# Kernel optimization log

Measured on AMD Instinct MI355X. Metric: run time of the kernel, lower is better.

## Reference

```python
import jax, jax.numpy as jnp
import numpy as np

EPS = 1e-12  # F.normalize default eps


def _l2_normalize(x, axis):
    n = jnp.sqrt(jnp.sum(x * x, axis=axis, keepdims=True))
    return x / jnp.maximum(n, EPS)


def setup_inputs() -> dict:
    key = jax.random.key(0)
    k1, k2 = jax.random.split(key)
    code = jax.random.normal(k1, (8, 768, 32, 32), dtype=jnp.float32)
    clusters = jax.random.normal(k2, (64, 768), dtype=jnp.float32)
    return {"code": code, "clusters": clusters, "image_hw": 512}


def reference(code, clusters, image_hw):
    # L2-normalize cluster centroids over channel dim and features over C
    normed_clusters = _l2_normalize(clusters, axis=1)            # [N, C]
    normed_features = _l2_normalize(code, axis=1)                # [B, C, H, W]
    # cosine similarity to every cluster
    inner_products = jnp.einsum('bchw,nc->bnhw', normed_features, normed_clusters)  # [B,N,H,W]
    # hard nearest-cluster assignment -> one-hot over N (channel axis 1)
    assign = jnp.argmax(inner_products, axis=1)                  # [B, H, W] int
    n_classes = clusters.shape[0]
    cluster_probs = jnp.moveaxis(
        jax.nn.one_hot(assign, n_classes, dtype=jnp.float32), -1, 1)  # [B,N,H,W]
    # training loss: negative mean of selected (max) similarity
    cluster_loss = -jnp.mean(jnp.sum(cluster_probs * inner_products, axis=1))
    # resize_to(cluster_probs, image): bilinear upsample to image resolution
    B, N = cluster_probs.shape[0], cluster_probs.shape[1]
    resized = jax.image.resize(cluster_probs, (B, N, image_hw, image_hw), method='bilinear')
    return (cluster_loss, resized, code)
```

## Files before the change

### kernel.cpp

```cpp
#include <hip/hip_runtime.h>

#define CCH 768
#define NCL 64
#define HWIN 1024
#define RES_ELEMS 134217728LL
#define CODE_ELEMS 6291456LL
#define CQUADS 1572863LL
#define COPY_BLOCKS 1536
#define DENSE_BLOCKS 2048

__global__ __launch_bounds__(256) void k_norm(const float* __restrict__ clusters,
                                              const float* __restrict__ code,
                                              float* __restrict__ nc_t,
                                              float* __restrict__ out)
{
    int tid = threadIdx.x;
    int n = blockIdx.x;
    __shared__ float red[256];
    float v0 = clusters[n * CCH + tid];
    float v1 = clusters[n * CCH + tid + 256];
    float v2 = clusters[n * CCH + tid + 512];
    red[tid] = v0 * v0 + v1 * v1 + v2 * v2;
    __syncthreads();
    for (int off = 128; off > 0; off >>= 1) {
        if (tid < off) red[tid] += red[tid + off];
        __syncthreads();
    }
    float scale = 1.0f / fmaxf(sqrtf(red[0]), 1e-12f);
    nc_t[(tid      ) * NCL + n] = v0 * scale;
    nc_t[(tid + 256) * NCL + n] = v1 * scale;
    nc_t[(tid + 512) * NCL + n] = v2 * scale;
    if (n == 0 && tid == 0) {
        out[0] = 0.0f;
        out[RES_ELEMS + 1] = code[0];
        out[RES_ELEMS + 2] = code[1];
        out[RES_ELEMS + 3] = code[2];
        out[RES_ELEMS + CODE_ELEMS] = code[CODE_ELEMS - 1];
    }
}

__global__ __launch_bounds__(256) void k_assign(const float* __restrict__ code,
                                                const float* __restrict__ nc_t,
                                                int* __restrict__ assign,
                                                float* __restrict__ out)
{
    __shared__ float lds_nc[64 * 64];
    __shared__ float lds_red[8 * 2048];
    __shared__ float lds_sq[8 * 32];

    int tid = threadIdx.x;
    int blk = blockIdx.x;
    int cg = tid >> 5;
    int ng = (tid >> 3) & 3;
    int pg = tid & 7;
    int b = blk >> 5;
    int pixb = (blk & 31) << 5;
    const float* codeB = code + (size_t)b * CCH * HWIN + pixb + (pg << 2);

    float acc[4][16];
    #pragma unroll
    for (int p = 0; p < 4; ++p)
        #pragma unroll
        for (int q = 0; q < 16; ++q) acc[p][q] = 0.f;
    float sq0 = 0.f, sq1 = 0.f, sq2 = 0.f, sq3 = 0.f;

    for (int k = 0; k < 12; ++k) {
        __syncthreads();
        const float4* src = (const float4*)(nc_t + k * 4096);
        float4* dst = (float4*)lds_nc;
        #pragma unroll
        for (int i = 0; i < 4; ++i) dst[tid + 256 * i] = src[tid + 256 * i];
        __syncthreads();
        #pragma unroll
        for (int m = 0; m < 8; ++m) {
            int ch = k * 64 + cg * 8 + m;
            float4 f = *(const float4*)(codeB + ch * HWIN);
            sq0 += f.x * f.x; sq1 += f.y * f.y; sq2 += f.z * f.z; sq3 += f.w * f.w;
            const float* ncrow = lds_nc + ((cg * 8 + m) << 6) + (ng << 4);
            #pragma unroll
            for (int q = 0; q < 16; ++q) {
                float w = ncrow[q];
                acc[0][q] += f.x * w;
                acc[1][q] += f.y * w;
                acc[2][q] += f.z * w;
                acc[3][q] += f.w * w;
            }
        }
    }

    #pragma unroll
    for (int p = 0; p < 4; ++p) {
        float4* dstp = (float4*)&lds_red[cg * 2048 + (pg * 4 + p) * 64 + ng * 16];
        dstp[0] = make_float4(acc[p][0],  acc[p][1],  acc[p][2],  acc[p][3]);
        dstp[1] = make_float4(acc[p][4],  acc[p][5],  acc[p][6],  acc[p][7]);
        dstp[2] = make_float4(acc[p][8],  acc[p][9],  acc[p][10], acc[p][11]);
        dstp[3] = make_float4(acc[p][12], acc[p][13], acc[p][14], acc[p][15]);
    }
    if (ng == 0) {
        lds_sq[cg * 32 + pg * 4 + 0] = sq0;
        lds_sq[cg * 32 + pg * 4 + 1] = sq1;
        lds_sq[cg * 32 + pg * 4 + 2] = sq2;
        lds_sq[cg * 32 + pg * 4 + 3] = sq3;
    }
    __syncthreads();

    for (int idx = tid; idx < 2048; idx += 256) {
        float s = 0.f;
        #pragma unroll
        for (int c2 = 0; c2 < 8; ++c2) s += lds_red[c2 * 2048 + idx];
        lds_nc[idx] = s;
    }
    __syncthreads();

    if (tid < 32) {
        float ss = 0.f;
        #pragma unroll
        for (int c2 = 0; c2 < 8; ++c2) ss += lds_sq[c2 * 32 + tid];
        float inv = 1.0f / fmaxf(sqrtf(ss), 1e-12f);
        float best = -1e30f; int bi = 0;
        for (int n = 0; n < 64; ++n) {
            float v = lds_nc[tid * 64 + n];
            if (v > best) { best = v; bi = n; }
        }
        assign[blk * 32 + tid] = bi;
        float l = best * inv;
        l += __shfl_down(l, 16);
        l += __shfl_down(l, 8);
        l += __shfl_down(l, 4);
        l += __shfl_down(l, 2);
        l += __shfl_down(l, 1);
        if (tid == 0) atomicAdd(out, -l * (1.0f / 8192.0f));
    }
}

__global__ __launch_bounds__(256) void k_dense(const int* __restrict__ assign,
                                               const float* __restrict__ code,
                                               float* __restrict__ out)
{
    int tid = threadIdx.x;
    int blk = blockIdx.x;

    if (blk >= DENSE_BLOCKS) {
        long long u = (long long)(blk - DENSE_BLOCKS) * 256 + tid;
        #pragma unroll
        for (int k = 0; k < 4; ++k) {
            long long q = u + (long long)k * (COPY_BLOCKS * 256);
            if (q < CQUADS) {
                const float* src = code + 3 + 4 * q;
                float4 v = make_float4(src[0], src[1], src[2], src[3]);
                *(float4*)(out + RES_ELEMS + 4 + 4 * q) = v;
            }
        }
        return;
    }

    int b =  blk >> 8;
    int n = (blk >> 2) & 63;
    int c =  blk & 3;
    int I0 = c << 7;
    int rbase = (I0 >> 4) - 1;

    __shared__ unsigned s_mask[10];
    __shared__ int4   s_jj[128];
    __shared__ float4 s_fj[128];

    int lane = tid & 63;
    int w = tid >> 6;

    {
        int r = (w << 1) + (lane >> 5);
        int ir = rbase + r; ir = ir < 0 ? 0 : (ir > 31 ? 31 : ir);
        bool pred = assign[(b << 10) + (ir << 5) + (lane & 31)] == n;
        unsigned long long m = __ballot(pred);
        if (lane == 0) { s_mask[(w << 1)] = (unsigned)m; s_mask[(w << 1) + 1] = (unsigned)(m >> 32); }
    }
    if (w == 0) {
        int r = 8 + (lane >> 5);
        int ir = rbase + r; ir = ir < 0 ? 0 : (ir > 31 ? 31 : ir);
        bool pred = assign[(b << 10) + (ir << 5) + (lane & 31)] == n;
        unsigned long long m = __ballot(pred);
        if (lane == 0) { s_mask[8] = (unsigned)m; s_mask[9] = (unsigned)(m >> 32); }
    }

    if (tid < 128) {
        int s = tid;
        int jl[4];
        if (s == 0) { jl[0] = 0; jl[1] = 1; jl[2] = 2; jl[3] = 511; }
        else { jl[0] = 4 * s - 1; jl[1] = 4 * s; jl[2] = 4 * s + 1; jl[3] = 4 * s + 2; }
        int pj[4]; float fjv[4];
        #pragma unroll
        for (int k = 0; k < 4; ++k) {
            int j = jl[k];
            float xj = (j + 0.5f) * 0.0625f - 0.5f;
            float fjf = floorf(xj);
            int jj = (int)fjf;
            fjv[k] = xj - fjf;
            int j0 = jj < 0 ? 0 : jj;
            int j1 = (jj + 1) > 31 ? 31 : (jj + 1);
            pj[k] = j0 | (j1 << 8);
        }
        s_jj[s] = make_int4(pj[0], pj[1], pj[2], pj[3]);
        s_fj[s] = make_float4(fjv[0], fjv[1], fjv[2], fjv[3]);
    }
    __syncthreads();

    int rr = tid >> 7;
    int s  = tid & 127;
    int4   pj4 = s_jj[s];
    float4 fj4 = s_fj[s];
    int   j0a[4] = { pj4.x & 255, pj4.y & 255, pj4.z & 255, pj4.w & 255 };
    int   j1a[4] = { pj4.x >> 8,  pj4.y >> 8,  pj4.z >> 8,  pj4.w >> 8 };
    float fja[4] = { fj4.x, fj4.y, fj4.z, fj4.w };

    long long planebase = 1LL + ((long long)b << 24) + ((long long)n << 18);

    for (int r2 = 0; r2 < 64; ++r2) {
        int i = I0 + (r2 << 1) + rr;
        float xi = (i + 0.5f) * 0.0625f - 0.5f;
        float fif = floorf(xi);
        int ii = (int)fif;
        float fi = xi - fif;
        float fi1 = 1.0f - fi;
        unsigned m0 = s_mask[ii - rbase];
        unsigned m1 = s_mask[ii - rbase + 1];
        float v[4];
        #pragma unroll
        for (int k = 0; k < 4; ++k) {
            float b00 = (float)((m0 >> j0a[k]) & 1u);
            float b01 = (float)((m0 >> j1a[k]) & 1u);
            float b10 = (float)((m1 >> j0a[k]) & 1u);
            float b11 = (float)((m1 >> j1a[k]) & 1u);
            float P = fi1 * b00 + fi * b10;
            float Q = fi1 * b01 + fi * b11;
            v[k] = P + fja[k] * (Q - P);
        }
        float* rowbase = out + planebase + ((long long)i << 9);
        if (s == 0) {
            rowbase[0] = v[0]; rowbase[1] = v[1]; rowbase[2] = v[2]; rowbase[511] = v[3];
        } else {
            *(float4*)(rowbase + 4 * s - 1) = make_float4(v[0], v[1], v[2], v[3]);
        }
    }
}

extern "C" void kernel_launch(void* const* d_in, const int* in_sizes, int n_in,
                              void* d_out, int out_size, void* d_ws, size_t ws_size,
                              hipStream_t stream)
{
    const float* code     = (const float*)d_in[0];
    const float* clusters = (const float*)d_in[1];
    float* out = (float*)d_out;
    float* nc_t = (float*)d_ws;
    int* assign = (int*)((char*)d_ws + 196608);

    k_norm  <<<NCL,                        256, 0, stream>>>(clusters, code, nc_t, out);
    k_assign<<<256,                        256, 0, stream>>>(code, nc_t, assign, out);
    k_dense <<<DENSE_BLOCKS + COPY_BLOCKS, 256, 0, stream>>>(assign, code, out);
}
```

Before: 618.6 us.

## Fuse cluster normalization into assign kernel and move code copy there

Removes the separate normalization kernel: each assign block computes the cluster norms itself and writes scaled, transposed cluster tiles straight into LDS. The code passthrough copy moves from the dense upsample kernel into extra blocks of the assign kernel, so it overlaps the underused assign phase. The loss atomicAdd becomes per-block partials that are summed deterministically in dense block 0. This saves a kernel launch but makes every assign block recompute the norms and use strided LDS stores.

```diff
diff --git a/kernel.cpp b/kernel.cpp
--- a/kernel.cpp
+++ b/kernel.cpp
@@ -6,50 +6,62 @@
 #define RES_ELEMS 134217728LL
 #define CODE_ELEMS 6291456LL
 #define CQUADS 1572863LL
-#define COPY_BLOCKS 1536
+#define ASSIGN_BLOCKS 256
+#define COPY_BLOCKS2 512
 #define DENSE_BLOCKS 2048
 
-__global__ __launch_bounds__(256) void k_norm(const float* __restrict__ clusters,
-                                              const float* __restrict__ code,
-                                              float* __restrict__ nc_t,
-                                              float* __restrict__ out)
+__global__ __launch_bounds__(256) void k_assign(const float* __restrict__ code,
+                                                const float* __restrict__ clusters,
+                                                int* __restrict__ assign,
+                                                float* __restrict__ loss_part,
+                                                float* __restrict__ out)
 {
     int tid = threadIdx.x;
-    int n = blockIdx.x;
-    __shared__ float red[256];
-    float v0 = clusters[n * CCH + tid];
-    float v1 = clusters[n * CCH + tid + 256];
-    float v2 = clusters[n * CCH + tid + 512];
-    red[tid] = v0 * v0 + v1 * v1 + v2 * v2;
-    __syncthreads();
-    for (int off = 128; off > 0; off >>= 1) {
-        if (tid < off) red[tid] += red[tid + off];
-        __syncthreads();
-    }
-    float scale = 1.0f / fmaxf(sqrtf(red[0]), 1e-12f);
-    nc_t[(tid      ) * NCL + n] = v0 * scale;
-    nc_t[(tid + 256) * NCL + n] = v1 * scale;
-    nc_t[(tid + 512) * NCL + n] = v2 * scale;
-    if (n == 0 && tid == 0) {
-        out[0] = 0.0f;
-        out[RES_ELEMS + 1] = code[0];
-        out[RES_ELEMS + 2] = code[1];
-        out[RES_ELEMS + 3] = code[2];
-        out[RES_ELEMS + CODE_ELEMS] = code[CODE_ELEMS - 1];
-    }
-}
-
-__global__ __launch_bounds__(256) void k_assign(const float* __restrict__ code,
-                                                const float* __restrict__ nc_t,
-                                                int* __restrict__ assign,
-                                                float* __restrict__ out)
-{
+    int blk = blockIdx.x;
+
+    if (blk >= ASSIGN_BLOCKS) {
+        long long u = (long long)(blk - ASSIGN_BLOCKS) * 256 + tid;
+        #pragma unroll
+        for (int k = 0; k < 12; ++k) {
+            long long q = u + (long long)k * (COPY_BLOCKS2 * 256);
+            if (q < CQUADS) {
+                const float* src = code + 3 + 4 * q;
+                float4 v = make_float4(src[0], src[1], src[2], src[3]);
+                *(float4*)(out + RES_ELEMS + 4 + 4 * q) = v;
+            }
+        }
+        if (blk == ASSIGN_BLOCKS && tid == 0) {
+            out[RES_ELEMS + 1] = code[0];
+            out[RES_ELEMS + 2] = code[1];
+            out[RES_ELEMS + 3] = code[2];
+            out[RES_ELEMS + CODE_ELEMS] = code[CODE_ELEMS - 1];
+        }
+        return;
+    }
+
     __shared__ float lds_nc[64 * 64];
     __shared__ float lds_red[8 * 2048];
     __shared__ float lds_sq[8 * 32];
-
-    int tid = threadIdx.x;
-    int blk = blockIdx.x;
+    __shared__ float s_scale[64];
+
+    int lane = tid & 63;
+    int w = tid >> 6;
+
+    for (int t = 0; t < 16; ++t) {
+        int n = w * 16 + t;
+        const float* row = clusters + n * CCH;
+        float ss = 0.f;
+        #pragma unroll
+        for (int j = 0; j < 3; ++j) {
+            float4 v = *(const float4*)(row + 4 * (lane + 64 * j));
+            ss += v.x * v.x + v.y * v.y + v.z * v.z + v.w * v.w;
+        }
+        #pragma unroll
+        for (int m = 1; m < 64; m <<= 1) ss += __shfl_xor(ss, m);
+        if (lane == 0) s_scale[n] = 1.0f / fmaxf(sqrtf(ss), 1e-12f);
+    }
+    __syncthreads();
+
     int cg = tid >> 5;
     int ng = (tid >> 3) & 3;
     int pg = tid & 7;
@@ -57,6 +69,10 @@
     int pixb = (blk & 31) << 5;
     const float* codeB = code + (size_t)b * CCH * HWIN + pixb + (pg << 2);
 
+    int n2 = tid >> 2;
+    int qq = tid & 3;
+    float myscale = s_scale[n2];
+
     float acc[4][16];
     #pragma unroll
     for (int p = 0; p < 4; ++p)
@@ -66,10 +82,15 @@
 
     for (int k = 0; k < 12; ++k) {
         __syncthreads();
-        const float4* src = (const float4*)(nc_t + k * 4096);
-        float4* dst = (float4*)lds_nc;
-        #pragma unroll
-        for (int i = 0; i < 4; ++i) dst[tid + 256 * i] = src[tid + 256 * i];
+        const float* srcrow = clusters + n2 * CCH + k * 64 + qq * 16;
+        #pragma unroll
+        for (int i = 0; i < 4; ++i) {
+            float4 v = *(const float4*)(srcrow + 4 * i);
+            lds_nc[(qq * 16 + 4 * i + 0) * 64 + n2] = v.x * myscale;
+            lds_nc[(qq * 16 + 4 * i + 1) * 64 + n2] = v.y * myscale;
+            lds_nc[(qq * 16 + 4 * i + 2) * 64 + n2] = v.z * myscale;
+            lds_nc[(qq * 16 + 4 * i + 3) * 64 + n2] = v.w * myscale;
+        }
         __syncthreads();
         #pragma unroll
         for (int m = 0; m < 8; ++m) {
@@ -79,11 +100,11 @@
             const float* ncrow = lds_nc + ((cg * 8 + m) << 6) + (ng << 4);
             #pragma unroll
             for (int q = 0; q < 16; ++q) {
-                float w = ncrow[q];
-                acc[0][q] += f.x * w;
-                acc[1][q] += f.y * w;
-                acc[2][q] += f.z * w;
-                acc[3][q] += f.w * w;
+                float w2 = ncrow[q];
+                acc[0][q] += f.x * w2;
+                acc[1][q] += f.y * w2;
+                acc[2][q] += f.z * w2;
+                acc[3][q] += f.w * w2;
             }
         }
     }
@@ -129,29 +150,25 @@
         l += __shfl_down(l, 4);
         l += __shfl_down(l, 2);
         l += __shfl_down(l, 1);
-        if (tid == 0) atomicAdd(out, -l * (1.0f / 8192.0f));
+        if (tid == 0) loss_part[blk] = -l * (1.0f / 8192.0f);
     }
 }
 
 __global__ __launch_bounds__(256) void k_dense(const int* __restrict__ assign,
-                                               const float* __restrict__ code,
+                                               const float* __restrict__ loss_part,
                                                float* __restrict__ out)
 {
     int tid = threadIdx.x;
     int blk = blockIdx.x;
 
-    if (blk >= DENSE_BLOCKS) {
-        long long u = (long long)(blk - DENSE_BLOCKS) * 256 + tid;
-        #pragma unroll
-        for (int k = 0; k < 4; ++k) {
-            long long q = u + (long long)k * (COPY_BLOCKS * 256);
-            if (q < CQUADS) {
-                const float* src = code + 3 + 4 * q;
-                float4 v = make_float4(src[0], src[1], src[2], src[3]);
-                *(float4*)(out + RES_ELEMS + 4 + 4 * q) = v;
-            }
-        }
-        return;
+    if (blk == 0) {
+        __shared__ float lr[4];
+        float v = loss_part[tid];
+        #pragma unroll
+        for (int m = 1; m < 64; m <<= 1) v += __shfl_xor(v, m);
+        if ((tid & 63) == 0) lr[tid >> 6] = v;
+        __syncthreads();
+        if (tid == 0) out[0] = lr[0] + lr[1] + lr[2] + lr[3];
     }
 
     int b =  blk >> 8;
@@ -250,10 +267,9 @@
     const float* code     = (const float*)d_in[0];
     const float* clusters = (const float*)d_in[1];
     float* out = (float*)d_out;
-    float* nc_t = (float*)d_ws;
-    int* assign = (int*)((char*)d_ws + 196608);
-
-    k_norm  <<<NCL,                        256, 0, stream>>>(clusters, code, nc_t, out);
-    k_assign<<<256,                        256, 0, stream>>>(code, nc_t, assign, out);
-    k_dense <<<DENSE_BLOCKS + COPY_BLOCKS, 256, 0, stream>>>(assign, code, out);
+    int* assign = (int*)d_ws;
+    float* loss_part = (float*)((char*)d_ws + 32768);
+
+    k_assign<<<ASSIGN_BLOCKS + COPY_BLOCKS2, 256, 0, stream>>>(code, clusters, assign, loss_part, out);
+    k_dense <<<DENSE_BLOCKS,                 256, 0, stream>>>(assign, loss_part, out);
 }
```

New measurement: 618.7 us. Within noise of the previous version (+0.0%).
